# Kernel optimization log

Hardware: AMD Instinct MI355X
Metric: run time of the kernel (lower is better)

The kernel has to match this reference:

```python
import jax, jax.numpy as jnp
import numpy as np

B, S, D = 4, 4096, 2048
ND = 64        # noise_dim
E = 3          # num_noise_types
LN_EPS = 1e-5


def setup_inputs() -> dict:
    key = jax.random.key(0)
    ks = jax.random.split(key, 20)
    sc = 0.02
    inp = {
        "x": jax.random.normal(ks[0], (B, S, D), jnp.float32),
        "eps": jax.random.normal(ks[1], (B, S, ND), jnp.float32),
        # noise-type classifier: D -> D//2 -> E
        "cls_w1": jax.random.normal(ks[2], (D, D // 2), jnp.float32) * sc,
        "cls_b1": jnp.zeros((D // 2,), jnp.float32),
        "cls_w2": jax.random.normal(ks[3], (D // 2, E), jnp.float32) * sc,
        "cls_b2": jnp.zeros((E,), jnp.float32),
        # variability predictor: D -> D//2 -> 1 (sigmoid)
        "var_w1": jax.random.normal(ks[4], (D, D // 2), jnp.float32) * sc,
        "var_b1": jnp.zeros((D // 2,), jnp.float32),
        "var_w2": jax.random.normal(ks[5], (D // 2, 1), jnp.float32) * sc,
        "var_b2": jnp.zeros((1,), jnp.float32),
        # per-expert encoders: D -> ND (SiLU) -> 2*ND
        "enc_w1": jax.random.normal(ks[6], (E, D, ND), jnp.float32) * sc,
        "enc_b1": jnp.zeros((E, ND), jnp.float32),
        "enc_w2": jax.random.normal(ks[7], (E, ND, 2 * ND), jnp.float32) * sc,
        "enc_b2": jnp.zeros((E, 2 * ND), jnp.float32),
        # per-expert decoders: ND -> D (SiLU) -> D, then LayerNorm
        "dec_w1": jax.random.normal(ks[8], (E, ND, D), jnp.float32) * sc,
        "dec_b1": jnp.zeros((E, D), jnp.float32),
        "dec_w2": jax.random.normal(ks[9], (E, D, D), jnp.float32) * sc,
        "dec_b2": jnp.zeros((E, D), jnp.float32),
        "ln_g": jnp.ones((E, D), jnp.float32),
        "ln_b": jnp.zeros((E, D), jnp.float32),
    }
    return inp


def reference(x, eps, cls_w1, cls_b1, cls_w2, cls_b2, var_w1, var_b1, var_w2,
              var_b2, enc_w1, enc_b1, enc_w2, enc_b2, dec_w1, dec_b1, dec_w2,
              dec_b2, ln_g, ln_b):
    # router: per-token argmax over classifier logits (softmax is monotone)
    logits = jax.nn.silu(x @ cls_w1 + cls_b1) @ cls_w2 + cls_b2      # [B,S,E]
    sel = jax.nn.one_hot(jnp.argmax(logits, axis=-1), E, dtype=x.dtype)  # [B,S,E]
    # per-token noise strength in (0,1)
    strength = jax.nn.sigmoid(jax.nn.silu(x @ var_w1 + var_b1) @ var_w2 + var_b2)  # [B,S,1]
    # encode with all E (small) experts, then select per token
    h = jax.nn.silu(jnp.einsum('bsd,edn->ebsn', x, enc_w1) + enc_b1[:, None, None, :])
    p = jnp.einsum('ebsn,enk->ebsk', h, enc_w2) + enc_b2[:, None, None, :]  # [E,B,S,2*ND]
    mean_all, logvar_all = jnp.split(p, 2, axis=-1)
    mean = jnp.einsum('ebsn,bse->bsn', mean_all, sel)                 # [B,S,ND]
    log_var = jnp.einsum('ebsn,bse->bsn', logvar_all, sel)
    # reparameterization
    noise = eps * jnp.exp(0.5 * log_var) + mean                        # [B,S,ND]
    # decode with all E experts, select per token
    dh = jax.nn.silu(jnp.einsum('bsn,end->ebsd', noise, dec_w1) + dec_b1[:, None, None, :])
    do = jnp.einsum('ebsd,edk->ebsk', dh, dec_w2) + dec_b2[:, None, None, :]  # [E,B,S,D]
    mu = jnp.mean(do, axis=-1, keepdims=True)
    var = jnp.mean(jnp.square(do - mu), axis=-1, keepdims=True)
    dn = (do - mu) * jax.lax.rsqrt(var + LN_EPS)
    do = dn * ln_g[:, None, None, :] + ln_b[:, None, None, :]
    decoded = jnp.einsum('ebsd,bse->bsd', do, sel)                    # [B,S,D]
    out = x + strength * decoded
    return out, noise, mean, log_var
```

## Files before the change

### kernel.cpp

```cpp
#include <hip/hip_runtime.h>
#include <hip/hip_bf16.h>

#define TOK 16384
#define DD  2048
#define HH  1024
#define NDIM 64
#define NOISE_OFF 33554432
#define MEAN_OFF  34603008
#define LV_OFF    35651584

#define WS_WCH  0u
#define WS_WCL  4194304u
#define WS_WVH  8388608u
#define WS_WD   12582912u
#define WS_W1T  37748736u
#define WS_LOGP 38535168u
#define WS_VARP 41680896u
#define WS_STR  42729472u
#define WS_CNT  42795008u
#define WS_LIST 42795264u
#define WS_NZ   42991872u

typedef float f32x4 __attribute__((ext_vector_type(4)));
typedef short short8 __attribute__((ext_vector_type(8)));

__device__ __forceinline__ f32x4 MFMA(uint4 a, uint4 b, f32x4 c) {
  return __builtin_amdgcn_mfma_f32_16x16x32_bf16(
      __builtin_bit_cast(short8, a), __builtin_bit_cast(short8, b), c, 0, 0, 0);
}

__device__ __forceinline__ unsigned short f2b(float f) {
  __hip_bfloat16 h = __float2bfloat16(f);
  return __builtin_bit_cast(unsigned short, h);
}
__device__ __forceinline__ float b2f(unsigned short u) {
  return __bfloat162float(__builtin_bit_cast(__hip_bfloat16, u));
}
__device__ __forceinline__ float siluf(float h) { return h / (1.f + expf(-h)); }

__global__ __launch_bounds__(256) void t_router_w(
    const float* __restrict__ cls_w1, const float* __restrict__ var_w1,
    unsigned short* __restrict__ wch, unsigned short* __restrict__ wcl,
    unsigned short* __restrict__ wvh) {
  __shared__ float tile[32][33];
  int z = blockIdx.z;
  const float* src = z ? var_w1 : cls_w1;
  int k0 = blockIdx.x * 32, n0 = blockIdx.y * 32;
  int tid = threadIdx.x;
#pragma unroll
  for (int p = 0; p < 4; ++p) {
    int idx = tid + p * 256; int kk = idx >> 5, nn = idx & 31;
    tile[kk][nn] = src[(size_t)(k0 + kk) * HH + (n0 + nn)];
  }
  __syncthreads();
#pragma unroll
  for (int p = 0; p < 4; ++p) {
    int idx = tid + p * 256; int kk = idx & 31, nn = idx >> 5;
    float v = tile[kk][nn];
    size_t o = (size_t)(n0 + nn) * DD + (k0 + kk);
    unsigned short h = f2b(v);
    if (z == 0) { wch[o] = h; wcl[o] = f2b(v - b2f(h)); }
    else        { wvh[o] = h; }
  }
}

__global__ __launch_bounds__(256) void t_dec_w(
    const float* __restrict__ dec_w2, unsigned short* __restrict__ wd) {
  __shared__ float tile[32][33];
  int e = blockIdx.z;
  const float* src = dec_w2 + (size_t)e * DD * DD;
  unsigned short* dst = wd + (size_t)e * DD * DD;
  int k0 = blockIdx.x * 32, n0 = blockIdx.y * 32;
  int tid = threadIdx.x;
#pragma unroll
  for (int p = 0; p < 4; ++p) {
    int idx = tid + p * 256; int kk = idx >> 5, nn = idx & 31;
    tile[kk][nn] = src[(size_t)(k0 + kk) * DD + (n0 + nn)];
  }
  __syncthreads();
#pragma unroll
  for (int p = 0; p < 4; ++p) {
    int idx = tid + p * 256; int kk = idx & 31, nn = idx >> 5;
    dst[(size_t)(n0 + nn) * DD + (k0 + kk)] = f2b(tile[kk][nn]);
  }
}

__global__ __launch_bounds__(256) void t_dec_w1(
    const float* __restrict__ dec_w1, unsigned short* __restrict__ w1t) {
  __shared__ float tile[32][33];
  int e = blockIdx.z;
  const float* src = dec_w1 + (size_t)e * NDIM * DD;
  unsigned short* dst = w1t + (size_t)e * DD * NDIM;
  int k0 = blockIdx.x * 32, c0 = blockIdx.y * 32;
  int tid = threadIdx.x;
#pragma unroll
  for (int p = 0; p < 4; ++p) {
    int idx = tid + p * 256; int kk = idx >> 5, nn = idx & 31;
    tile[kk][nn] = src[(size_t)(k0 + kk) * DD + (c0 + nn)];
  }
  __syncthreads();
#pragma unroll
  for (int p = 0; p < 4; ++p) {
    int idx = tid + p * 256; int kk = idx & 31, nn = idx >> 5;
    dst[(size_t)(c0 + nn) * NDIM + (k0 + kk)] = f2b(tile[kk][nn]);
  }
}

__global__ __launch_bounds__(256, 2) void k_router(
    const float* __restrict__ x,
    const float* __restrict__ cls_b1, const float* __restrict__ cls_w2,
    const float* __restrict__ var_b1, const float* __restrict__ var_w2,
    const unsigned short* __restrict__ wch, const unsigned short* __restrict__ wcl,
    const unsigned short* __restrict__ wvh,
    float* __restrict__ logp, float* __restrict__ varp) {
  __shared__ unsigned short AH[64 * 32];
  __shared__ unsigned short AL[64 * 32];
  int bx = blockIdx.x;
  int mt = bx >> 2, nblk = bx & 3;
  int rowbase = mt * 64;
  int tid = threadIdx.x;
  int lane = tid & 63, wave = tid >> 6;
  int arl = lane & 15, kg = lane >> 4;
  int colw = nblk * 256 + wave * 64;
  f32x4 accC[4][4], accV[4][4];
#pragma unroll
  for (int a = 0; a < 4; ++a)
#pragma unroll
    for (int b = 0; b < 4; ++b) { accC[a][b] = (f32x4)0.f; accV[a][b] = (f32x4)0.f; }
  int srow = tid >> 2, ks = tid & 3;
  const float* xrow = x + (size_t)(rowbase + srow) * DD + ks * 8;
  unsigned short* wrH = &AH[srow * 32 + ks * 8];
  unsigned short* wrL = &AL[srow * 32 + ks * 8];

  for (int k0 = 0; k0 < DD; k0 += 32) {
    float4 v0 = *(const float4*)(xrow + k0);
    float4 v1 = *(const float4*)(xrow + k0 + 4);
    float vv[8] = {v0.x, v0.y, v0.z, v0.w, v1.x, v1.y, v1.z, v1.w};
    union { unsigned short u[8]; uint4 q; } ph, pl;
#pragma unroll
    for (int j = 0; j < 8; ++j) {
      unsigned short h = f2b(vv[j]);
      ph.u[j] = h;
      pl.u[j] = f2b(vv[j] - b2f(h));
    }
    *(uint4*)wrH = ph.q;
    *(uint4*)wrL = pl.q;
    __syncthreads();
    uint4 ah[4], al[4];
#pragma unroll
    for (int rt = 0; rt < 4; ++rt) {
      ah[rt] = *(const uint4*)&AH[(rt * 16 + arl) * 32 + kg * 8];
      al[rt] = *(const uint4*)&AL[(rt * 16 + arl) * 32 + kg * 8];
    }
#pragma unroll
    for (int nt = 0; nt < 4; ++nt) {
      int col = colw + nt * 16 + arl;
      size_t bo = (size_t)col * DD + k0 + kg * 8;
      uint4 bh = *(const uint4*)(wch + bo);
      uint4 bl = *(const uint4*)(wcl + bo);
      uint4 bv = *(const uint4*)(wvh + bo);
#pragma unroll
      for (int rt = 0; rt < 4; ++rt) {
        accC[rt][nt] = MFMA(ah[rt], bh, accC[rt][nt]);
        accC[rt][nt] = MFMA(al[rt], bh, accC[rt][nt]);
        accC[rt][nt] = MFMA(ah[rt], bl, accC[rt][nt]);
        accV[rt][nt] = MFMA(ah[rt], bv, accV[rt][nt]);
      }
    }
    __syncthreads();
  }

  float part[4][4][3], pv[4][4];
#pragma unroll
  for (int rt = 0; rt < 4; ++rt)
#pragma unroll
    for (int r = 0; r < 4; ++r) {
      part[rt][r][0] = 0.f; part[rt][r][1] = 0.f; part[rt][r][2] = 0.f;
      pv[rt][r] = 0.f;
    }
#pragma unroll
  for (int nt = 0; nt < 4; ++nt) {
    int colg = colw + nt * 16 + arl;
    float bbc = cls_b1[colg];
    float w0 = cls_w2[colg * 3 + 0];
    float w1v = cls_w2[colg * 3 + 1];
    float w2v = cls_w2[colg * 3 + 2];
    float bbv = var_b1[colg];
    float wv = var_w2[colg];
#pragma unroll
    for (int rt = 0; rt < 4; ++rt)
#pragma unroll
      for (int r = 0; r < 4; ++r) {
        float s = siluf(accC[rt][nt][r] + bbc);
        part[rt][r][0] += s * w0;
        part[rt][r][1] += s * w1v;
        part[rt][r][2] += s * w2v;
        pv[rt][r] += siluf(accV[rt][nt][r] + bbv) * wv;
      }
  }
  for (int m = 1; m < 16; m <<= 1)
#pragma unroll
    for (int rt = 0; rt < 4; ++rt)
#pragma unroll
      for (int r = 0; r < 4; ++r) {
        part[rt][r][0] += __shfl_xor(part[rt][r][0], m);
        part[rt][r][1] += __shfl_xor(part[rt][r][1], m);
        part[rt][r][2] += __shfl_xor(part[rt][r][2], m);
        pv[rt][r] += __shfl_xor(pv[rt][r], m);
      }
  if (arl == 0) {
    int slot = nblk * 4 + wave;
#pragma unroll
    for (int rt = 0; rt < 4; ++rt)
#pragma unroll
      for (int r = 0; r < 4; ++r) {
        int row = rowbase + rt * 16 + kg * 4 + r;
        size_t o = (size_t)slot * TOK + row;
        logp[o * 3 + 0] = part[rt][r][0];
        logp[o * 3 + 1] = part[rt][r][1];
        logp[o * 3 + 2] = part[rt][r][2];
        varp[o] = pv[rt][r];
      }
  }
}

__global__ __launch_bounds__(256) void k_select(
    const float* __restrict__ logp, const float* __restrict__ varp,
    const float* __restrict__ cls_b2, const float* __restrict__ var_b2,
    float* __restrict__ strength, int* __restrict__ cnt, int* __restrict__ list) {
  int t = blockIdx.x * 256 + threadIdx.x;
  if (t >= TOK) return;
  float l0 = cls_b2[0], l1 = cls_b2[1], l2 = cls_b2[2];
  float vv = var_b2[0];
#pragma unroll
  for (int s = 0; s < 16; ++s) {
    size_t o = (size_t)s * TOK + t;
    l0 += logp[o * 3 + 0];
    l1 += logp[o * 3 + 1];
    l2 += logp[o * 3 + 2];
    vv += varp[o];
  }
  int best = 0; float bl = l0;
  if (l1 > bl) { best = 1; bl = l1; }
  if (l2 > bl) { best = 2; bl = l2; }
  int pos = atomicAdd(&cnt[best], 1);
  list[best * TOK + pos] = t;
  strength[t] = 1.f / (1.f + expf(-vv));
}

__global__ __launch_bounds__(256) void k_encode(
    const float* __restrict__ x, const float* __restrict__ eps,
    const float* __restrict__ enc_w1, const float* __restrict__ enc_b1,
    const float* __restrict__ enc_w2, const float* __restrict__ enc_b2,
    const int* __restrict__ cnt, const int* __restrict__ list,
    float* __restrict__ out, unsigned short* __restrict__ nzbf) {
  __shared__ unsigned short xl[8][2048];
  __shared__ float part[4][512];
  __shared__ float hls[8][64];
  __shared__ float pls[8][128];
  __shared__ int toks[8];
  __shared__ int es[8];
  int tid = threadIdx.x;
  if (tid < 8) {
    int slot = blockIdx.x * 8 + tid;
    int c0 = cnt[0], c1 = cnt[1];
    int e, idx;
    if (slot < c0)            { e = 0; idx = slot; }
    else if (slot < c0 + c1)  { e = 1; idx = slot - c0; }
    else                      { e = 2; idx = slot - c0 - c1; }
    toks[tid] = list[e * TOK + idx];
    es[tid] = e;
  }
  __syncthreads();
  bool uni = true;
  int e0 = es[0];
#pragma unroll
  for (int r = 1; r < 8; ++r) uni = uni && (es[r] == e0);
#pragma unroll
  for (int r = 0; r < 8; ++r) {
    const float4* xr = (const float4*)(x + (size_t)toks[r] * DD);
#pragma unroll
    for (int i = 0; i < 2; ++i) {
      int kq = tid + i * 256;
      float4 v = xr[kq];
      union { unsigned short u[4]; unsigned long long q; } p;
      p.u[0] = f2b(v.x); p.u[1] = f2b(v.y); p.u[2] = f2b(v.z); p.u[3] = f2b(v.w);
      *(unsigned long long*)(&xl[r][kq * 4]) = p.q;
    }
  }
  __syncthreads();
  int n = tid & 63, q = tid >> 6;
  float acc[8];
#pragma unroll
  for (int r = 0; r < 8; ++r) acc[r] = 0.f;
  if (uni) {
    const float* w = enc_w1 + (size_t)e0 * DD * NDIM;
    for (int kk = 0; kk < 512; ++kk) {
      int k = q * 512 + kk;
      float wv = w[k * NDIM + n];
#pragma unroll
      for (int r = 0; r < 8; ++r) acc[r] += b2f(xl[r][k]) * wv;
    }
  } else {
#pragma unroll
    for (int r = 0; r < 8; ++r) {
      const float* w = enc_w1 + (size_t)es[r] * DD * NDIM;
      float a = 0.f;
      for (int kk = 0; kk < 512; ++kk) {
        int k = q * 512 + kk;
        a += b2f(xl[r][k]) * w[k * NDIM + n];
      }
      acc[r] = a;
    }
  }
#pragma unroll
  for (int r = 0; r < 8; ++r) part[q][r * 64 + n] = acc[r];
  __syncthreads();
#pragma unroll
  for (int it = 0; it < 2; ++it) {
    int o = tid + it * 256; int r = o >> 6, n2 = o & 63; int e = es[r];
    float h = part[0][o] + part[1][o] + part[2][o] + part[3][o] + enc_b1[e * 64 + n2];
    hls[r][n2] = siluf(h);
  }
  __syncthreads();
#pragma unroll
  for (int it = 0; it < 4; ++it) {
    int o = tid + it * 256; int r = o >> 7, j = o & 127; int e = es[r];
    const float* w2 = enc_w2 + e * 64 * 128;
    float a = 0.f;
#pragma unroll
    for (int nn = 0; nn < 64; ++nn) a += hls[r][nn] * w2[nn * 128 + j];
    pls[r][j] = a + enc_b2[e * 128 + j];
  }
  __syncthreads();
#pragma unroll
  for (int it = 0; it < 2; ++it) {
    int o = tid + it * 256; int r = o >> 6, j = o & 63; int t = toks[r];
    float m = pls[r][j], lv = pls[r][64 + j];
    float nz = eps[(size_t)t * 64 + j] * expf(0.5f * lv) + m;
    out[NOISE_OFF + (size_t)t * 64 + j] = nz;
    out[MEAN_OFF + (size_t)t * 64 + j] = m;
    out[LV_OFF + (size_t)t * 64 + j] = lv;
    nzbf[t * 64 + j] = f2b(nz);
  }
}

__global__ __launch_bounds__(512, 2) void k_decode(
    const float* __restrict__ x,
    const float* __restrict__ dec_b1, const float* __restrict__ dec_b2,
    const float* __restrict__ ln_g, const float* __restrict__ ln_b,
    const unsigned short* __restrict__ w1t, const unsigned short* __restrict__ wd,
    const unsigned short* __restrict__ nzbf,
    const int* __restrict__ cnt, const int* __restrict__ list,
    const float* __restrict__ strength, float* __restrict__ out) {
  int bx = blockIdx.x;
  int x7 = bx & 7;
  int e = (x7 * 3) >> 3;
  int idx = x7 - (e == 0 ? 0 : (e == 1 ? 3 : 6));
  int we = (e == 2) ? 2 : 3;
  int mt = (bx >> 3) * we + idx;
  int cnte = cnt[e];
  int base = mt * 32;
  if (base >= cnte) return;
  __shared__ unsigned short dhs[65536];
  __shared__ unsigned short nzs[2048];
  __shared__ float sums[32][2];
  __shared__ int tokv[32];
  __shared__ int vld[32];
  int tid = threadIdx.x;
  int lane = tid & 63, wave = tid >> 6;
  int arl = lane & 15, kg = lane >> 4;
  int colbase = wave * 256;
  if (tid < 32) {
    int s = base + tid;
    int ok = (s < cnte) ? 1 : 0;
    vld[tid] = ok;
    tokv[tid] = list[e * TOK + (ok ? s : base)];
  }
  __syncthreads();
#pragma unroll
  for (int i = 0; i < 4; ++i) {
    int o = tid + i * 512; int r = o >> 6, k = o & 63;
    nzs[(k >> 5) * 1024 + r * 32 + (k & 31)] = nzbf[(size_t)tokv[r] * 64 + k];
  }
  __syncthreads();
  const unsigned short* w1e = w1t + (size_t)e * DD * NDIM;
  const float* b1 = dec_b1 + (size_t)e * DD;
  float b1v[16];
#pragma unroll
  for (int nt = 0; nt < 16; ++nt) b1v[nt] = b1[colbase + nt * 16 + arl];
  {
    f32x4 acch[2][16];
#pragma unroll
    for (int rt = 0; rt < 2; ++rt)
#pragma unroll
      for (int nt = 0; nt < 16; ++nt) acch[rt][nt] = (f32x4)0.f;
#pragma unroll
    for (int h = 0; h < 2; ++h) {
      uint4 a0 = *(const uint4*)&nzs[h * 1024 + arl * 32 + kg * 8];
      uint4 a1 = *(const uint4*)&nzs[h * 1024 + (16 + arl) * 32 + kg * 8];
#pragma unroll
      for (int nt = 0; nt < 16; ++nt) {
        int col = colbase + nt * 16 + arl;
        uint4 b = *(const uint4*)(w1e + (size_t)col * NDIM + h * 32 + kg * 8);
        acch[0][nt] = MFMA(a0, b, acch[0][nt]);
        acch[1][nt] = MFMA(a1, b, acch[1][nt]);
      }
    }
#pragma unroll
    for (int rt = 0; rt < 2; ++rt)
#pragma unroll
      for (int nt = 0; nt < 16; ++nt) {
        int c = colbase + nt * 16 + arl;
#pragma unroll
        for (int r = 0; r < 4; ++r) {
          int row = rt * 16 + kg * 4 + r;
          float s = siluf(acch[rt][nt][r] + b1v[nt]);
          dhs[(c >> 5) * 1024 + row * 32 + (c & 31)] = f2b(s);
        }
      }
  }
  __syncthreads();
  const unsigned short* Bt = wd + (size_t)e * DD * DD;
  f32x4 acc[2][16];
#pragma unroll
  for (int rt = 0; rt < 2; ++rt)
#pragma unroll
    for (int nt = 0; nt < 16; ++nt) acc[rt][nt] = (f32x4)0.f;
  for (int k0 = 0; k0 < DD; k0 += 32) {
    int tilo = (k0 >> 5) * 1024;
    uint4 af0 = *(const uint4*)&dhs[tilo + arl * 32 + kg * 8];
    uint4 af1 = *(const uint4*)&dhs[tilo + (16 + arl) * 32 + kg * 8];
    int kb = k0 + kg * 8;
#pragma unroll
    for (int nt = 0; nt < 16; ++nt) {
      int col = colbase + nt * 16 + arl;
      uint4 b = *(const uint4*)(Bt + (size_t)col * DD + kb);
      acc[0][nt] = MFMA(af0, b, acc[0][nt]);
      acc[1][nt] = MFMA(af1, b, acc[1][nt]);
    }
  }
  __syncthreads();
  if (tid < 64) sums[tid >> 1][tid & 1] = 0.f;
  __syncthreads();
  const float* b2 = dec_b2 + (size_t)e * DD;
  float s1[2][4], s2[2][4];
#pragma unroll
  for (int rt = 0; rt < 2; ++rt)
#pragma unroll
    for (int r = 0; r < 4; ++r) { s1[rt][r] = 0.f; s2[rt][r] = 0.f; }
#pragma unroll
  for (int nt = 0; nt < 16; ++nt) {
    int col = colbase + nt * 16 + arl;
    float bbv = b2[col];
#pragma unroll
    for (int rt = 0; rt < 2; ++rt)
#pragma unroll
      for (int r = 0; r < 4; ++r) {
        float v = acc[rt][nt][r] + bbv;
        acc[rt][nt][r] = v;
        s1[rt][r] += v;
        s2[rt][r] += v * v;
      }
  }
  for (int m = 1; m < 16; m <<= 1)
#pragma unroll
    for (int rt = 0; rt < 2; ++rt)
#pragma unroll
      for (int r = 0; r < 4; ++r) {
        s1[rt][r] += __shfl_xor(s1[rt][r], m);
        s2[rt][r] += __shfl_xor(s2[rt][r], m);
      }
  if (arl == 0) {
#pragma unroll
    for (int rt = 0; rt < 2; ++rt)
#pragma unroll
      for (int r = 0; r < 4; ++r) {
        int row = rt * 16 + kg * 4 + r;
        atomicAdd(&sums[row][0], s1[rt][r]);
        atomicAdd(&sums[row][1], s2[rt][r]);
      }
  }
  __syncthreads();
  float mu[2][4], rs[2][4], strv[2][4]; size_t xoff[2][4]; int okr[2][4];
#pragma unroll
  for (int rt = 0; rt < 2; ++rt)
#pragma unroll
    for (int r = 0; r < 4; ++r) {
      int row = rt * 16 + kg * 4 + r;
      float m1 = sums[row][0] * (1.f / 2048.f);
      float var = sums[row][1] * (1.f / 2048.f) - m1 * m1;
      mu[rt][r] = m1;
      rs[rt][r] = rsqrtf(var + 1e-5f);
      int t = tokv[row];
      okr[rt][r] = vld[row];
      strv[rt][r] = strength[t];
      xoff[rt][r] = (size_t)t * DD;
    }
#pragma unroll
  for (int nt = 0; nt < 16; ++nt) {
    int col = colbase + nt * 16 + arl;
    float g = ln_g[e * DD + col], bv = ln_b[e * DD + col];
#pragma unroll
    for (int rt = 0; rt < 2; ++rt)
#pragma unroll
      for (int r = 0; r < 4; ++r) {
        if (okr[rt][r]) {
          float nvv = (acc[rt][nt][r] - mu[rt][r]) * rs[rt][r];
          out[xoff[rt][r] + col] = x[xoff[rt][r] + col] + strv[rt][r] * (nvv * g + bv);
        }
      }
  }
}

extern "C" void kernel_launch(void* const* d_in, const int* in_sizes, int n_in,
                              void* d_out, int out_size, void* d_ws, size_t ws_size,
                              hipStream_t stream) {
  const float* x      = (const float*)d_in[0];
  const float* eps    = (const float*)d_in[1];
  const float* cls_w1 = (const float*)d_in[2];
  const float* cls_b1 = (const float*)d_in[3];
  const float* cls_w2 = (const float*)d_in[4];
  const float* cls_b2 = (const float*)d_in[5];
  const float* var_w1 = (const float*)d_in[6];
  const float* var_b1 = (const float*)d_in[7];
  const float* var_w2 = (const float*)d_in[8];
  const float* var_b2 = (const float*)d_in[9];
  const float* enc_w1 = (const float*)d_in[10];
  const float* enc_b1 = (const float*)d_in[11];
  const float* enc_w2 = (const float*)d_in[12];
  const float* enc_b2 = (const float*)d_in[13];
  const float* dec_w1 = (const float*)d_in[14];
  const float* dec_b1 = (const float*)d_in[15];
  const float* dec_w2 = (const float*)d_in[16];
  const float* dec_b2 = (const float*)d_in[17];
  const float* ln_g   = (const float*)d_in[18];
  const float* ln_b   = (const float*)d_in[19];
  float* out = (float*)d_out;
  char* ws = (char*)d_ws;
  unsigned short* wch  = (unsigned short*)(ws + WS_WCH);
  unsigned short* wcl  = (unsigned short*)(ws + WS_WCL);
  unsigned short* wvh  = (unsigned short*)(ws + WS_WVH);
  unsigned short* wd   = (unsigned short*)(ws + WS_WD);
  unsigned short* w1t  = (unsigned short*)(ws + WS_W1T);
  float* logp = (float*)(ws + WS_LOGP);
  float* varp = (float*)(ws + WS_VARP);
  float* str  = (float*)(ws + WS_STR);
  int* cnt    = (int*)(ws + WS_CNT);
  int* list   = (int*)(ws + WS_LIST);
  unsigned short* nzbf = (unsigned short*)(ws + WS_NZ);

  hipMemsetAsync(ws + WS_CNT, 0, 256, stream);

  hipLaunchKernelGGL(t_router_w, dim3(64, 32, 2), dim3(256), 0, stream,
                     cls_w1, var_w1, wch, wcl, wvh);
  hipLaunchKernelGGL(t_dec_w, dim3(64, 64, 3), dim3(256), 0, stream, dec_w2, wd);
  hipLaunchKernelGGL(t_dec_w1, dim3(2, 64, 3), dim3(256), 0, stream, dec_w1, w1t);
  hipLaunchKernelGGL(k_router, dim3(1024), dim3(256), 0, stream,
                     x, cls_b1, cls_w2, var_b1, var_w2, wch, wcl, wvh, logp, varp);
  hipLaunchKernelGGL(k_select, dim3(64), dim3(256), 0, stream,
                     logp, varp, cls_b2, var_b2, str, cnt, list);
  hipLaunchKernelGGL(k_encode, dim3(2048), dim3(256), 0, stream,
                     x, eps, enc_w1, enc_b1, enc_w2, enc_b2, cnt, list, out, nzbf);
  hipLaunchKernelGGL(k_decode, dim3(2048), dim3(512), 0, stream,
                     x, dec_b1, dec_b2, ln_g, ln_b, w1t, wd, nzbf, cnt, list, str, out);
}
```

Baseline: 1.986 ms.

## Split decoder into staged hidden-activation, tiled GEMM and LayerNorm kernels

When the workspace is large enough, the fused decoder is replaced by three kernels. The first materializes the SiLU hidden activations in bf16 into a padded, expert-grouped global buffer. The second runs a 128x256-tiled, double-buffered GEMM that uses global_load_lds and writes partial LayerNorm statistics. The third applies LayerNorm and the residual. The router kernel also moves to 512-thread blocks covering 128 rows, so each weight load is reused across more rows. The cost is extra global traffic for the hidden buffer and the pre-norm output round trip, plus a workspace-size-dependent code path.

```diff
diff --git a/kernel.cpp b/kernel.cpp
--- a/kernel.cpp
+++ b/kernel.cpp
@@ -9,17 +9,33 @@
 #define MEAN_OFF  34603008
 #define LV_OFF    35651584
 
-#define WS_WCH  0u
-#define WS_WCL  4194304u
-#define WS_WVH  8388608u
-#define WS_WD   12582912u
-#define WS_W1T  37748736u
-#define WS_LOGP 38535168u
-#define WS_VARP 41680896u
-#define WS_STR  42729472u
-#define WS_CNT  42795008u
-#define WS_LIST 42795264u
-#define WS_NZ   42991872u
+#define WS_DHG   0u
+#define WS_WCH   0u
+#define WS_WCL   4194304u
+#define WS_WVH   8388608u
+#define WS_LOGP  12582912u
+#define WS_VARP  15728640u
+#define WS_WD    70254592u
+#define WS_W1T   95420416u
+#define WS_STR   96206848u
+#define WS_CNT   96272384u
+#define WS_LIST  96272640u
+#define WS_NZ    96469248u
+#define WS_ROWOF 98566400u
+#define WS_PARTS 98631936u
+#define WS_NEED  103022848u
+
+#define WO_WCH  0u
+#define WO_WCL  4194304u
+#define WO_WVH  8388608u
+#define WO_WD   12582912u
+#define WO_W1T  37748736u
+#define WO_LOGP 38535168u
+#define WO_VARP 41680896u
+#define WO_STR  42729472u
+#define WO_CNT  42795008u
+#define WO_LIST 42795264u
+#define WO_NZ   42991872u
 
 typedef float f32x4 __attribute__((ext_vector_type(4)));
 typedef short short8 __attribute__((ext_vector_type(8)));
@@ -27,6 +43,12 @@
 __device__ __forceinline__ f32x4 MFMA(uint4 a, uint4 b, f32x4 c) {
   return __builtin_amdgcn_mfma_f32_16x16x32_bf16(
       __builtin_bit_cast(short8, a), __builtin_bit_cast(short8, b), c, 0, 0, 0);
+}
+
+__device__ __forceinline__ void gload16(const void* g, void* l) {
+  __builtin_amdgcn_global_load_lds(
+      (const __attribute__((address_space(1))) unsigned int*)g,
+      (__attribute__((address_space(3))) unsigned int*)l, 16, 0, 0);
 }
 
 __device__ __forceinline__ unsigned short f2b(float f) {
@@ -106,22 +128,24 @@
   }
 }
 
-__global__ __launch_bounds__(256, 2) void k_router(
+__global__ __launch_bounds__(512) void k_router(
     const float* __restrict__ x,
     const float* __restrict__ cls_b1, const float* __restrict__ cls_w2,
     const float* __restrict__ var_b1, const float* __restrict__ var_w2,
     const unsigned short* __restrict__ wch, const unsigned short* __restrict__ wcl,
     const unsigned short* __restrict__ wvh,
     float* __restrict__ logp, float* __restrict__ varp) {
-  __shared__ unsigned short AH[64 * 32];
-  __shared__ unsigned short AL[64 * 32];
+  __shared__ uint4 AHq[512];
+  __shared__ uint4 ALq[512];
   int bx = blockIdx.x;
-  int mt = bx >> 2, nblk = bx & 3;
-  int rowbase = mt * 64;
+  int nblk = (bx & 7) >> 1;
+  int mt = ((bx >> 3) << 1) | (bx & 1);
+  int rowbase = mt * 128;
   int tid = threadIdx.x;
   int lane = tid & 63, wave = tid >> 6;
+  int wn = wave & 3, wm = wave >> 2;
   int arl = lane & 15, kg = lane >> 4;
-  int colw = nblk * 256 + wave * 64;
+  int colw = nblk * 256 + wn * 64;
   f32x4 accC[4][4], accV[4][4];
 #pragma unroll
   for (int a = 0; a < 4; ++a)
@@ -129,8 +153,7 @@
     for (int b = 0; b < 4; ++b) { accC[a][b] = (f32x4)0.f; accV[a][b] = (f32x4)0.f; }
   int srow = tid >> 2, ks = tid & 3;
   const float* xrow = x + (size_t)(rowbase + srow) * DD + ks * 8;
-  unsigned short* wrH = &AH[srow * 32 + ks * 8];
-  unsigned short* wrL = &AL[srow * 32 + ks * 8];
+  int wslot = (srow >> 4) * 64 + ks * 16 + (srow & 15);
 
   for (int k0 = 0; k0 < DD; k0 += 32) {
     float4 v0 = *(const float4*)(xrow + k0);
@@ -143,14 +166,15 @@
       ph.u[j] = h;
       pl.u[j] = f2b(vv[j] - b2f(h));
     }
-    *(uint4*)wrH = ph.q;
-    *(uint4*)wrL = pl.q;
+    AHq[wslot] = ph.q;
+    ALq[wslot] = pl.q;
     __syncthreads();
     uint4 ah[4], al[4];
 #pragma unroll
     for (int rt = 0; rt < 4; ++rt) {
-      ah[rt] = *(const uint4*)&AH[(rt * 16 + arl) * 32 + kg * 8];
-      al[rt] = *(const uint4*)&AL[(rt * 16 + arl) * 32 + kg * 8];
+      int slot = (wm * 4 + rt) * 64 + kg * 16 + arl;
+      ah[rt] = AHq[slot];
+      al[rt] = ALq[slot];
     }
 #pragma unroll
     for (int nt = 0; nt < 4; ++nt) {
@@ -209,12 +233,12 @@
         pv[rt][r] += __shfl_xor(pv[rt][r], m);
       }
   if (arl == 0) {
-    int slot = nblk * 4 + wave;
+    int slot = nblk * 4 + wn;
 #pragma unroll
     for (int rt = 0; rt < 4; ++rt)
 #pragma unroll
       for (int r = 0; r < 4; ++r) {
-        int row = rowbase + rt * 16 + kg * 4 + r;
+        int row = rowbase + wm * 64 + rt * 16 + kg * 4 + r;
         size_t o = (size_t)slot * TOK + row;
         logp[o * 3 + 0] = part[rt][r][0];
         logp[o * 3 + 1] = part[rt][r][1];
@@ -345,7 +369,228 @@
   }
 }
 
-__global__ __launch_bounds__(512, 2) void k_decode(
+__global__ __launch_bounds__(512) void k_dh(
+    const unsigned short* __restrict__ w1t, const float* __restrict__ dec_b1,
+    const unsigned short* __restrict__ nzbf,
+    const int* __restrict__ cnt, const int* __restrict__ list,
+    unsigned short* __restrict__ dhg, int* __restrict__ rowOf) {
+  __shared__ unsigned short dhs[65536];
+  __shared__ unsigned short nzs[2048];
+  __shared__ int tokv[32];
+  int tid = threadIdx.x;
+  int r0 = blockIdx.x * 32;
+  int c0 = cnt[0], c1 = cnt[1], c2 = cnt[2];
+  int tb1 = (c0 + 127) & ~127;
+  int tb2 = tb1 + ((c1 + 127) & ~127);
+  int e, lbase, cd;
+  if (r0 < tb1)      { e = 0; lbase = r0;       cd = c0; }
+  else if (r0 < tb2) { e = 1; lbase = r0 - tb1; cd = c1; }
+  else               { e = 2; lbase = r0 - tb2; cd = c2; }
+  if (tid < 32) {
+    int idx = lbase + tid;
+    int ok = idx < cd && idx >= 0;
+    int t = ok ? list[e * TOK + idx] : -1;
+    tokv[tid] = t;
+    if (ok) rowOf[t] = r0 + tid;
+  }
+  __syncthreads();
+#pragma unroll
+  for (int i = 0; i < 4; ++i) {
+    int o = tid + i * 512; int r = o >> 6, k = o & 63;
+    int t = tokv[r];
+    nzs[(k >> 5) * 1024 + r * 32 + (k & 31)] =
+        (t >= 0) ? nzbf[(size_t)t * 64 + k] : (unsigned short)0;
+  }
+  __syncthreads();
+  int lane = tid & 63, wave = tid >> 6;
+  int arl = lane & 15, kg = lane >> 4;
+  int colbase = wave * 256;
+  const unsigned short* w1e = w1t + (size_t)e * DD * NDIM;
+  const float* b1 = dec_b1 + (size_t)e * DD;
+  float b1v[16];
+#pragma unroll
+  for (int nt = 0; nt < 16; ++nt) b1v[nt] = b1[colbase + nt * 16 + arl];
+  f32x4 acch[2][16];
+#pragma unroll
+  for (int rt = 0; rt < 2; ++rt)
+#pragma unroll
+    for (int nt = 0; nt < 16; ++nt) acch[rt][nt] = (f32x4)0.f;
+#pragma unroll
+  for (int h = 0; h < 2; ++h) {
+    uint4 a0 = *(const uint4*)&nzs[h * 1024 + arl * 32 + kg * 8];
+    uint4 a1 = *(const uint4*)&nzs[h * 1024 + (16 + arl) * 32 + kg * 8];
+#pragma unroll
+    for (int nt = 0; nt < 16; ++nt) {
+      int col = colbase + nt * 16 + arl;
+      uint4 b = *(const uint4*)(w1e + (size_t)col * NDIM + h * 32 + kg * 8);
+      acch[0][nt] = MFMA(a0, b, acch[0][nt]);
+      acch[1][nt] = MFMA(a1, b, acch[1][nt]);
+    }
+  }
+#pragma unroll
+  for (int rt = 0; rt < 2; ++rt)
+#pragma unroll
+    for (int nt = 0; nt < 16; ++nt) {
+      int c = colbase + nt * 16 + arl;
+#pragma unroll
+      for (int r = 0; r < 4; ++r) {
+        int row = rt * 16 + kg * 4 + r;
+        float s = siluf(acch[rt][nt][r] + b1v[nt]);
+        dhs[(c >> 5) * 1024 + row * 32 + (c & 31)] = f2b(s);
+      }
+    }
+  __syncthreads();
+#pragma unroll
+  for (int it = 0; it < 16; ++it) {
+    int idx = tid + it * 512;
+    int row = idx >> 8, ks8 = idx & 255;
+    int k = ks8 * 8;
+    uint4 v = *(const uint4*)&dhs[(k >> 5) * 1024 + row * 32 + (k & 31)];
+    *(uint4*)&dhg[(size_t)(r0 + row) * DD + k] = v;
+  }
+}
+
+__global__ __launch_bounds__(512) void k_gemm(
+    const unsigned short* __restrict__ dhg, const unsigned short* __restrict__ wd,
+    const float* __restrict__ dec_b2,
+    const int* __restrict__ cnt, const int* __restrict__ list,
+    float* __restrict__ out, float* __restrict__ parts) {
+  __shared__ uint4 As4[2][512];
+  __shared__ uint4 Bs4[2][1024];
+  __shared__ int tokv[128];
+  int tid = threadIdx.x;
+  int bx = blockIdx.x;
+  int nslice = bx & 7, tile = bx >> 3;
+  int c0 = cnt[0], c1 = cnt[1], c2 = cnt[2];
+  int t0 = (c0 + 127) >> 7, t1 = (c1 + 127) >> 7, t2 = (c2 + 127) >> 7;
+  if (tile >= t0 + t1 + t2) return;
+  int e, lbase, cd;
+  if (tile < t0)           { e = 0; lbase = tile * 128;             cd = c0; }
+  else if (tile < t0 + t1) { e = 1; lbase = (tile - t0) * 128;      cd = c1; }
+  else                     { e = 2; lbase = (tile - t0 - t1) * 128; cd = c2; }
+  int rp0 = tile * 128;
+  if (tid < 128) {
+    int idx = lbase + tid;
+    tokv[tid] = (idx < cd) ? list[e * TOK + idx] : -1;
+  }
+  const unsigned short* Ag = dhg + (size_t)rp0 * DD;
+  const unsigned short* Bg = wd + (size_t)e * DD * DD + (size_t)(nslice * 256) * DD;
+  int lane = tid & 63, wave = tid >> 6;
+  int wm = wave >> 2, wn = wave & 3;
+  int arl = lane & 15, kg = lane >> 4;
+  int srA = ((tid >> 6) << 4) | (tid & 15);
+  int skA = (tid >> 4) & 3;
+#define STAGE(h, k0)                                                         \
+  {                                                                          \
+    gload16(Ag + (size_t)srA * DD + (k0) + skA * 8,                          \
+            (char*)&As4[h][0] + tid * 16);                                   \
+    gload16(Bg + (size_t)srA * DD + (k0) + skA * 8,                          \
+            (char*)&Bs4[h][0] + tid * 16);                                   \
+    gload16(Bg + (size_t)(srA + 128) * DD + (k0) + skA * 8,                  \
+            (char*)&Bs4[h][0] + (tid + 512) * 16);                           \
+  }
+  f32x4 acc[4][4];
+#pragma unroll
+  for (int mt = 0; mt < 4; ++mt)
+#pragma unroll
+    for (int nt = 0; nt < 4; ++nt) acc[mt][nt] = (f32x4)0.f;
+  STAGE(0, 0);
+  __syncthreads();
+  for (int t = 0; t < 64; ++t) {
+    int cur = t & 1;
+    if (t < 63) STAGE(cur ^ 1, (t + 1) * 32);
+    uint4 bfr[4];
+#pragma unroll
+    for (int nt = 0; nt < 4; ++nt)
+      bfr[nt] = Bs4[cur][(wn * 4 + nt) * 64 + kg * 16 + arl];
+#pragma unroll
+    for (int mt = 0; mt < 4; ++mt) {
+      uint4 afr = As4[cur][(wm * 4 + mt) * 64 + kg * 16 + arl];
+#pragma unroll
+      for (int nt = 0; nt < 4; ++nt)
+        acc[mt][nt] = MFMA(afr, bfr[nt], acc[mt][nt]);
+    }
+    __syncthreads();
+  }
+#undef STAGE
+  const float* b2 = dec_b2 + (size_t)e * DD + nslice * 256;
+  float b2v[4];
+#pragma unroll
+  for (int nt = 0; nt < 4; ++nt) b2v[nt] = b2[wn * 64 + nt * 16 + arl];
+  int sl = (nslice * 4 + wn) * 2;
+#pragma unroll
+  for (int mt = 0; mt < 4; ++mt) {
+#pragma unroll
+    for (int rr = 0; rr < 4; ++rr) {
+      int row = wm * 64 + mt * 16 + kg * 4 + rr;
+      int token = tokv[row];
+      float s1 = 0.f, s2 = 0.f;
+      float v[4];
+#pragma unroll
+      for (int nt = 0; nt < 4; ++nt) {
+        v[nt] = acc[mt][nt][rr] + b2v[nt];
+        s1 += v[nt];
+        s2 += v[nt] * v[nt];
+      }
+      if (token >= 0) {
+        size_t o = (size_t)token * DD + nslice * 256 + wn * 64 + arl;
+#pragma unroll
+        for (int nt = 0; nt < 4; ++nt) out[o + nt * 16] = v[nt];
+      }
+#pragma unroll
+      for (int m = 1; m < 16; m <<= 1) {
+        s1 += __shfl_xor(s1, m);
+        s2 += __shfl_xor(s2, m);
+      }
+      if (arl == 0) {
+        size_t po = (size_t)(rp0 + row) * 64 + sl;
+        parts[po] = s1;
+        parts[po + 1] = s2;
+      }
+    }
+  }
+}
+
+__global__ __launch_bounds__(256) void k_ln(
+    const float* __restrict__ x, const float* __restrict__ ln_g,
+    const float* __restrict__ ln_b, const float* __restrict__ strength,
+    const int* __restrict__ rowOf, const float* __restrict__ parts,
+    const int* __restrict__ cnt, float* __restrict__ out) {
+  int wave = threadIdx.x >> 6, lane = threadIdx.x & 63;
+  int t = blockIdx.x * 4 + wave;
+  int rp = rowOf[t];
+  int c0 = cnt[0], c1 = cnt[1];
+  int tb1 = (c0 + 127) & ~127;
+  int tb2 = tb1 + ((c1 + 127) & ~127);
+  int e = rp < tb1 ? 0 : (rp < tb2 ? 1 : 2);
+  float s1 = 0.f, s2 = 0.f;
+#pragma unroll
+  for (int i = 0; i < 32; ++i) {
+    s1 += parts[(size_t)rp * 64 + i * 2];
+    s2 += parts[(size_t)rp * 64 + i * 2 + 1];
+  }
+  float mu = s1 * (1.f / 2048.f);
+  float var = s2 * (1.f / 2048.f) - mu * mu;
+  float rs = rsqrtf(var + 1e-5f);
+  float str = strength[t];
+  size_t o = (size_t)t * DD;
+#pragma unroll
+  for (int i = 0; i < 8; ++i) {
+    int col = i * 256 + lane * 4;
+    float4 v = *(const float4*)&out[o + col];
+    float4 xv = *(const float4*)&x[o + col];
+    float4 g = *(const float4*)&ln_g[(size_t)e * DD + col];
+    float4 b = *(const float4*)&ln_b[(size_t)e * DD + col];
+    float4 r;
+    r.x = xv.x + str * ((v.x - mu) * rs * g.x + b.x);
+    r.y = xv.y + str * ((v.y - mu) * rs * g.y + b.y);
+    r.z = xv.z + str * ((v.z - mu) * rs * g.z + b.z);
+    r.w = xv.w + str * ((v.w - mu) * rs * g.w + b.w);
+    *(float4*)&out[o + col] = r;
+  }
+}
+
+__global__ __launch_bounds__(512, 2) void k_decode_old(
     const float* __restrict__ x,
     const float* __restrict__ dec_b1, const float* __restrict__ dec_b2,
     const float* __restrict__ ln_g, const float* __restrict__ ln_b,
@@ -492,10 +737,10 @@
       float var = sums[row][1] * (1.f / 2048.f) - m1 * m1;
       mu[rt][r] = m1;
       rs[rt][r] = rsqrtf(var + 1e-5f);
-      int t = tokv[row];
+      int tt = tokv[row];
       okr[rt][r] = vld[row];
-      strv[rt][r] = strength[t];
-      xoff[rt][r] = (size_t)t * DD;
+      strv[rt][r] = strength[tt];
+      xoff[rt][r] = (size_t)tt * DD;
     }
 #pragma unroll
   for (int nt = 0; nt < 16; ++nt) {
@@ -538,30 +783,44 @@
   const float* ln_b   = (const float*)d_in[19];
   float* out = (float*)d_out;
   char* ws = (char*)d_ws;
-  unsigned short* wch  = (unsigned short*)(ws + WS_WCH);
-  unsigned short* wcl  = (unsigned short*)(ws + WS_WCL);
-  unsigned short* wvh  = (unsigned short*)(ws + WS_WVH);
-  unsigned short* wd   = (unsigned short*)(ws + WS_WD);
-  unsigned short* w1t  = (unsigned short*)(ws + WS_W1T);
-  float* logp = (float*)(ws + WS_LOGP);
-  float* varp = (float*)(ws + WS_VARP);
-  float* str  = (float*)(ws + WS_STR);
-  int* cnt    = (int*)(ws + WS_CNT);
-  int* list   = (int*)(ws + WS_LIST);
-  unsigned short* nzbf = (unsigned short*)(ws + WS_NZ);
-
-  hipMemsetAsync(ws + WS_CNT, 0, 256, stream);
+  bool big = ws_size >= (size_t)WS_NEED;
+
+  unsigned short* wch  = (unsigned short*)(ws + (big ? WS_WCH  : WO_WCH));
+  unsigned short* wcl  = (unsigned short*)(ws + (big ? WS_WCL  : WO_WCL));
+  unsigned short* wvh  = (unsigned short*)(ws + (big ? WS_WVH  : WO_WVH));
+  unsigned short* wd   = (unsigned short*)(ws + (big ? WS_WD   : WO_WD));
+  unsigned short* w1t  = (unsigned short*)(ws + (big ? WS_W1T  : WO_W1T));
+  float* logp = (float*)(ws + (big ? WS_LOGP : WO_LOGP));
+  float* varp = (float*)(ws + (big ? WS_VARP : WO_VARP));
+  float* str  = (float*)(ws + (big ? WS_STR  : WO_STR));
+  int* cnt    = (int*)(ws + (big ? WS_CNT  : WO_CNT));
+  int* list   = (int*)(ws + (big ? WS_LIST : WO_LIST));
+  unsigned short* nzbf = (unsigned short*)(ws + (big ? WS_NZ : WO_NZ));
+
+  hipMemsetAsync(cnt, 0, 256, stream);
 
   hipLaunchKernelGGL(t_router_w, dim3(64, 32, 2), dim3(256), 0, stream,
                      cls_w1, var_w1, wch, wcl, wvh);
   hipLaunchKernelGGL(t_dec_w, dim3(64, 64, 3), dim3(256), 0, stream, dec_w2, wd);
   hipLaunchKernelGGL(t_dec_w1, dim3(2, 64, 3), dim3(256), 0, stream, dec_w1, w1t);
-  hipLaunchKernelGGL(k_router, dim3(1024), dim3(256), 0, stream,
+  hipLaunchKernelGGL(k_router, dim3(512), dim3(512), 0, stream,
                      x, cls_b1, cls_w2, var_b1, var_w2, wch, wcl, wvh, logp, varp);
   hipLaunchKernelGGL(k_select, dim3(64), dim3(256), 0, stream,
                      logp, varp, cls_b2, var_b2, str, cnt, list);
   hipLaunchKernelGGL(k_encode, dim3(2048), dim3(256), 0, stream,
                      x, eps, enc_w1, enc_b1, enc_w2, enc_b2, cnt, list, out, nzbf);
-  hipLaunchKernelGGL(k_decode, dim3(2048), dim3(512), 0, stream,
-                     x, dec_b1, dec_b2, ln_g, ln_b, w1t, wd, nzbf, cnt, list, str, out);
-}
+  if (big) {
+    unsigned short* dhg = (unsigned short*)(ws + WS_DHG);
+    int* rowOf = (int*)(ws + WS_ROWOF);
+    float* parts = (float*)(ws + WS_PARTS);
+    hipLaunchKernelGGL(k_dh, dim3(528), dim3(512), 0, stream,
+                       w1t, dec_b1, nzbf, cnt, list, dhg, rowOf);
+    hipLaunchKernelGGL(k_gemm, dim3(1048), dim3(512), 0, stream,
+                       dhg, wd, dec_b2, cnt, list, out, parts);
+    hipLaunchKernelGGL(k_ln, dim3(4096), dim3(256), 0, stream,
+                       x, ln_g, ln_b, str, rowOf, parts, cnt, out);
+  } else {
+    hipLaunchKernelGGL(k_decode_old, dim3(2048), dim3(512), 0, stream,
+                       x, dec_b1, dec_b2, ln_g, ln_b, w1t, wd, nzbf, cnt, list, str, out);
+  }
+}
```

After: 1.659 ms. 1.2x faster.
